# Performance work log

Measured on AMD Instinct MI355X. Metric: run time of the kernel, lower is better.

## Reference

```python
import jax, jax.numpy as jnp
import numpy as np

D_MODEL, D_K, D_V, D_H, SEQ = 1024, 64, 64, 16, 4096


def setup_inputs() -> dict:
    key = jax.random.key(0)
    ks = jax.random.split(key, 16)
    s = lambda fan_in: 1.0 / np.sqrt(fan_in)
    return {
        "X": jax.random.normal(ks[0], (SEQ, D_MODEL), jnp.float32),
        # shared Q/K/V projections (nn.Linear stores weight as [out, in])
        "Wq": jax.random.uniform(ks[1], (D_K, D_MODEL), jnp.float32, -s(D_MODEL), s(D_MODEL)),
        "bq": jax.random.uniform(ks[2], (D_K,), jnp.float32, -s(D_MODEL), s(D_MODEL)),
        "Wk": jax.random.uniform(ks[3], (D_K, D_MODEL), jnp.float32, -s(D_MODEL), s(D_MODEL)),
        "bk": jax.random.uniform(ks[4], (D_K,), jnp.float32, -s(D_MODEL), s(D_MODEL)),
        "Wv": jax.random.uniform(ks[5], (D_V, D_MODEL), jnp.float32, -s(D_MODEL), s(D_MODEL)),
        "bv": jax.random.uniform(ks[6], (D_V,), jnp.float32, -s(D_MODEL), s(D_MODEL)),
        # per-head linears stacked along head axis
        "Whq": jax.random.uniform(ks[7], (D_H, D_K, D_K), jnp.float32, -s(D_K), s(D_K)),
        "bhq": jax.random.uniform(ks[8], (D_H, D_K), jnp.float32, -s(D_K), s(D_K)),
        "Whk": jax.random.uniform(ks[9], (D_H, D_K, D_K), jnp.float32, -s(D_K), s(D_K)),
        "bhk": jax.random.uniform(ks[10], (D_H, D_K), jnp.float32, -s(D_K), s(D_K)),
        "Whv": jax.random.uniform(ks[11], (D_H, D_V, D_V), jnp.float32, -s(D_V), s(D_V)),
        "bhv": jax.random.uniform(ks[12], (D_H, D_V), jnp.float32, -s(D_V), s(D_V)),
        # final projection: d_h*d_v -> d_model
        "Wo": jax.random.uniform(ks[13], (D_MODEL, D_H * D_V), jnp.float32, -s(D_H * D_V), s(D_H * D_V)),
        "bo": jax.random.uniform(ks[14], (D_MODEL,), jnp.float32, -s(D_H * D_V), s(D_H * D_V)),
    }


def reference(X, Wq, bq, Wk, bk, Wv, bv, Whq, bhq, Whk, bhk, Whv, bhv, Wo, bo):
    # shared projections: [T, d_k] / [T, d_v]
    Q = X @ Wq.T + bq
    K = X @ Wk.T + bk
    V = X @ Wv.T + bv
    # per-head linears, all heads at once: [H, T, d_k]
    qh = jnp.einsum("tk,hjk->htj", Q, Whq) + bhq[:, None, :]
    kh = jnp.einsum("tk,hjk->htj", K, Whk) + bhk[:, None, :]
    vh = jnp.einsum("tv,hjv->htj", V, Whv) + bhv[:, None, :]
    # scaled dot-product attention per head: [H, T, T]
    scale = 1.0 / jnp.sqrt(jnp.asarray(Q.shape[-1], X.dtype))
    attn = jax.nn.softmax(jnp.einsum("htk,hsk->hts", qh, kh) * scale, axis=-1)
    rep = jnp.einsum("hts,hsv->htv", attn, vh)  # [H, T, d_v]
    # hstack heads -> [T, H*d_v], then final projection
    concat = rep.transpose(1, 0, 2).reshape(X.shape[0], -1)
    return concat @ Wo.T + bo
```

## Files before the change

kernel.cpp:

```cpp
#include <hip/hip_runtime.h>

#define T 4096
#define DM 1024
#define DK 64
#define H 16

typedef short s8 __attribute__((ext_vector_type(8)));
typedef float f4 __attribute__((ext_vector_type(4)));
typedef unsigned short us4 __attribute__((ext_vector_type(4)));
typedef unsigned u32x4 __attribute__((ext_vector_type(4)));
typedef __bf16 bf2 __attribute__((ext_vector_type(2)));

#define MFMA16(a,b,c) __builtin_amdgcn_mfma_f32_16x16x32_bf16((a),(b),(c),0,0,0)
#define SCALE_Q 0.18033688011112042f

__device__ __forceinline__ unsigned short f2bf(float x){
  __bf16 b = (__bf16)x;
  return __builtin_bit_cast(unsigned short, b);
}
__device__ __forceinline__ unsigned pk2(float a, float b){
  bf2 v; v[0] = (__bf16)a; v[1] = (__bf16)b;
  return __builtin_bit_cast(unsigned, v);
}

__device__ __forceinline__ void gload16(const void* g, void* lds){
  __builtin_amdgcn_global_load_lds((const __attribute__((address_space(1))) unsigned int*)g,
                                   (__attribute__((address_space(3))) unsigned int*)lds,
                                   16, 0, 0);
}

__device__ __forceinline__ void xch(unsigned X, unsigned Y, unsigned &E, unsigned &O){
#if __has_builtin(__builtin_amdgcn_permlane32_swap) && __has_builtin(__builtin_amdgcn_permlane16_swap)
  auto a = __builtin_amdgcn_permlane32_swap(X, Y, false, false);
  auto b = __builtin_amdgcn_permlane16_swap(a[0], a[1], false, false);
  E = b[0]; O = b[1];
#else
  int l = threadIdx.x & 63;
  int idxE = ((((l >> 4) & 1) * 32 + (l & 15))) << 2;
  unsigned eX = __builtin_amdgcn_ds_bpermute(idxE, X);
  unsigned eY = __builtin_amdgcn_ds_bpermute(idxE, Y);
  E = (l < 32) ? eX : eY;
  unsigned oX = __builtin_amdgcn_ds_bpermute(idxE + 64, X);
  unsigned oY = __builtin_amdgcn_ds_bpermute(idxE + 64, Y);
  O = (l < 32) ? oX : oY;
#endif
}

__global__ void cvt_bf16(const float* __restrict__ in, unsigned short* __restrict__ out, int n4){
  int i = blockIdx.x * blockDim.x + threadIdx.x;
  if (i >= n4) return;
  float4 v = reinterpret_cast<const float4*>(in)[i];
  us4 o;
  o[0] = f2bf(v.x); o[1] = f2bf(v.y); o[2] = f2bf(v.z); o[3] = f2bf(v.w);
  reinterpret_cast<us4*>(out)[i] = o;
}

#define N_WOB (DM * DM / 4)
#define N_W3  (64 * DM / 4)
#define N_WH  (16 * 64 * 64 / 4)
__global__ __launch_bounds__(256) void prep_all(
    const float* __restrict__ Wo,
    const float* __restrict__ Wq, const float* __restrict__ Wk, const float* __restrict__ Wv,
    const float* __restrict__ Whq, const float* __restrict__ Whk, const float* __restrict__ Whv,
    const float* __restrict__ bq, const float* __restrict__ bk, const float* __restrict__ bv,
    const float* __restrict__ bhq, const float* __restrict__ bhk, const float* __restrict__ bhv,
    unsigned short* __restrict__ Wob, unsigned short* __restrict__ W3b,
    unsigned short* __restrict__ Whb, float* __restrict__ beff){
  int idx = blockIdx.x * 256 + threadIdx.x;
  if (idx < N_WOB){
    float4 v = reinterpret_cast<const float4*>(Wo)[idx];
    us4 o; o[0]=f2bf(v.x); o[1]=f2bf(v.y); o[2]=f2bf(v.z); o[3]=f2bf(v.w);
    reinterpret_cast<us4*>(Wob)[idx] = o;
    return;
  }
  idx -= N_WOB;
  if (idx < 3 * N_W3){
    int seg = idx / N_W3, i = idx - seg * N_W3;
    const float* src = (seg == 0) ? Wq : ((seg == 1) ? Wk : Wv);
    float4 v = reinterpret_cast<const float4*>(src)[i];
    us4 o; o[0]=f2bf(v.x); o[1]=f2bf(v.y); o[2]=f2bf(v.z); o[3]=f2bf(v.w);
    reinterpret_cast<us4*>(W3b)[seg * N_W3 + i] = o;
    return;
  }
  idx -= 3 * N_W3;
  if (idx < 3 * N_WH){
    int seg = idx / N_WH, i = idx - seg * N_WH;
    const float* src = (seg == 0) ? Whq : ((seg == 1) ? Whk : Whv);
    float s = (seg == 0) ? SCALE_Q : 1.0f;
    float4 v = reinterpret_cast<const float4*>(src)[i];
    us4 o; o[0]=f2bf(v.x*s); o[1]=f2bf(v.y*s); o[2]=f2bf(v.z*s); o[3]=f2bf(v.w*s);
    reinterpret_cast<us4*>(Whb)[seg * N_WH + i] = o;
    return;
  }
  idx -= 3 * N_WH;
  if (idx < 3072){
    int seg = idx >> 10, j = idx & 1023;
    const float* Wh = (seg == 0) ? Whq : ((seg == 1) ? Whk : Whv);
    const float* b  = (seg == 0) ? bq  : ((seg == 1) ? bk  : bv);
    const float* bh = (seg == 0) ? bhq : ((seg == 1) ? bhk : bhv);
    float s = (seg == 0) ? SCALE_Q : 1.0f;
    const float* wr = Wh + j * 64;
    float acc = 0.f;
    #pragma unroll 8
    for (int k = 0; k < 64; ++k) acc += wr[k] * b[k];
    beff[idx] = (acc + bh[j]) * s;
  }
}

template<int MODE, int BM, int BN, int NT>
__global__ __launch_bounds__(256) void gemmX(const unsigned short* __restrict__ A,
                       const unsigned short* __restrict__ B,
                       const float* __restrict__ bias,
                       unsigned short* __restrict__ q_out,
                       unsigned short* __restrict__ k_out,
                       unsigned short* __restrict__ v_out,
                       float* __restrict__ f_out){
  __shared__ __align__(16) short la[2][BM * 64];
  __shared__ __align__(16) short lb[2][BN * 64];
  const int tid = threadIdx.x;
  const int wv = tid >> 6, l = tid & 63;
  const int lr = l & 15, lh = l >> 4;
  const int wr = wv >> 1, wc = wv & 1;
  const int tm = blockIdx.x / NT, tn = blockIdx.x % NT;
  const int t0 = tm * BM, o0 = tn * BN;
  constexpr int MF = BM / 32;
  constexpr int NF = BN / 32;
  constexpr int ACH = BM / 32;
  constexpr int BCH = BN / 32;
  constexpr int LAB = BM * 128;
  constexpr int LBB = BN * 128;

  f4 acc[MF][NF];
  #pragma unroll
  for (int i = 0; i < MF; ++i)
    #pragma unroll
    for (int j = 0; j < NF; ++j) acc[i][j] = (f4){0.f, 0.f, 0.f, 0.f};

  const int srow = tid >> 3;
  const int scs  = (tid & 7) ^ (srow & 7);
  const unsigned short* ap = A + (size_t)(t0 + srow) * DM + scs * 8;
  const unsigned short* bp = B + (size_t)(o0 + srow) * DM + scs * 8;
  char* ad = (char*)&la[0][0] + tid * 16;
  char* bd = (char*)&lb[0][0] + tid * 16;

  auto stage = [&](int BUF){
    #pragma unroll
    for (int i = 0; i < ACH; ++i)
      gload16(ap + (size_t)i * 32 * DM, ad + BUF * LAB + i * 4096);
    #pragma unroll
    for (int i = 0; i < BCH; ++i)
      gload16(bp + (size_t)i * 32 * DM, bd + BUF * LBB + i * 4096);
    ap += 64; bp += 64;
  };

  const int asw0 = (lh ^ (lr & 7)) * 16, asw1 = ((lh ^ 4) ^ (lr & 7)) * 16;
  const char* aB0 = (const char*)&la[0][0] + (wr * (BM / 2) + lr) * 128 + asw0;
  const char* aB1 = (const char*)&la[0][0] + (wr * (BM / 2) + lr) * 128 + asw1;
  const char* bB0 = (const char*)&lb[0][0] + (wc * (BN / 2) + lr) * 128 + asw0;
  const char* bB1 = (const char*)&lb[0][0] + (wc * (BN / 2) + lr) * 128 + asw1;

  auto step = [&](int BUF, bool dostage){
    if (dostage) stage(BUF ^ 1);
    s8 af[MF][2], bfr[NF][2];
    #pragma unroll
    for (int mf = 0; mf < MF; ++mf){
      af[mf][0] = *(const s8*)(aB0 + BUF * LAB + mf * 2048);
      af[mf][1] = *(const s8*)(aB1 + BUF * LAB + mf * 2048);
    }
    #pragma unroll
    for (int nf = 0; nf < NF; ++nf){
      bfr[nf][0] = *(const s8*)(bB0 + BUF * LBB + nf * 2048);
      bfr[nf][1] = *(const s8*)(bB1 + BUF * LBB + nf * 2048);
    }
    __builtin_amdgcn_s_setprio(1);
    #pragma unroll
    for (int mf = 0; mf < MF; ++mf)
      #pragma unroll
      for (int nf = 0; nf < NF; ++nf){
        acc[mf][nf] = MFMA16(af[mf][0], bfr[nf][0], acc[mf][nf]);
        acc[mf][nf] = MFMA16(af[mf][1], bfr[nf][1], acc[mf][nf]);
      }
    __builtin_amdgcn_s_setprio(0);
    __syncthreads();
  };

  stage(0);
  __syncthreads();
  #pragma unroll 1
  for (int t2 = 0; t2 < 8; ++t2){
    step(0, true);
    step(1, t2 < 7);
  }

  #pragma unroll
  for (int nf = 0; nf < NF; ++nf){
    int o = o0 + wc * (BN / 2) + nf * 16 + lr;
    float bs = (MODE == 4) ? 0.f : bias[o];
    int sel = o >> 6, oc = o & 63;
    unsigned short* yo = (sel == 0) ? q_out : ((sel == 1) ? k_out : v_out);
    #pragma unroll
    for (int mf = 0; mf < MF; ++mf)
      #pragma unroll
      for (int r = 0; r < 4; ++r){
        int t = t0 + wr * (BM / 2) + mf * 16 + lh * 4 + r;
        float v = acc[mf][nf][r] + bs;
        if (MODE == 2) f_out[(size_t)t * DM + o] = v;
        else           yo[(size_t)t * 64 + oc] = f2bf(v);
      }
  }
}

__global__ __launch_bounds__(256) void gemm_heads(const unsigned short* __restrict__ Yq,
                        const unsigned short* __restrict__ Yk,
                        const unsigned short* __restrict__ Yv,
                        const unsigned short* __restrict__ Whb,
                        const float* __restrict__ beff,
                        unsigned short* __restrict__ qhb,
                        unsigned short* __restrict__ khb,
                        unsigned short* __restrict__ vtb){
  const int tid = threadIdx.x;
  const int wv = tid >> 6, l = tid & 63;
  const int lr = l & 15, lh = l >> 4;
  const int rem = blockIdx.x % 48, tb = blockIdx.x / 48;
  const int kind = rem >> 4, h = rem & 15;
  const unsigned short* Y = (kind == 0) ? Yq : ((kind == 1) ? Yk : Yv);
  const unsigned short* B = Whb + (size_t)rem * 4096;
  const int t0 = tb * 256 + wv * 64;

  s8 wf[4][2], yf[4][2];
  #pragma unroll
  for (int nf = 0; nf < 4; ++nf)
    #pragma unroll
    for (int hf = 0; hf < 2; ++hf)
      wf[nf][hf] = *reinterpret_cast<const s8*>(B + (size_t)(nf * 16 + lr) * 64 + hf * 32 + lh * 8);
  #pragma unroll
  for (int mf = 0; mf < 4; ++mf)
    #pragma unroll
    for (int hf = 0; hf < 2; ++hf)
      yf[mf][hf] = *reinterpret_cast<const s8*>(Y + (size_t)(t0 + mf * 16 + lr) * 64 + hf * 32 + lh * 8);

  f4 acc[4][4];
  #pragma unroll
  for (int i = 0; i < 4; ++i)
    #pragma unroll
    for (int j = 0; j < 4; ++j) acc[i][j] = (f4){0.f, 0.f, 0.f, 0.f};

  if (kind < 2){
    #pragma unroll
    for (int mf = 0; mf < 4; ++mf)
      #pragma unroll
      for (int nf = 0; nf < 4; ++nf){
        acc[mf][nf] = MFMA16(yf[mf][0], wf[nf][0], acc[mf][nf]);
        acc[mf][nf] = MFMA16(yf[mf][1], wf[nf][1], acc[mf][nf]);
      }
    unsigned short* out = (kind == 0) ? qhb : khb;
    #pragma unroll
    for (int nf = 0; nf < 4; ++nf){
      int j = nf * 16 + lr;
      float bs = beff[rem * 64 + j];
      #pragma unroll
      for (int mf = 0; mf < 4; ++mf)
        #pragma unroll
        for (int r = 0; r < 4; ++r){
          int t = t0 + mf * 16 + lh * 4 + r;
          out[((size_t)h * T + t) * DK + j] = f2bf(acc[mf][nf][r] + bs);
        }
    }
  } else {
    #pragma unroll
    for (int nf = 0; nf < 4; ++nf)
      #pragma unroll
      for (int mf = 0; mf < 4; ++mf){
        acc[nf][mf] = MFMA16(wf[nf][0], yf[mf][0], acc[nf][mf]);
        acc[nf][mf] = MFMA16(wf[nf][1], yf[mf][1], acc[nf][mf]);
      }
    #pragma unroll
    for (int nf = 0; nf < 4; ++nf){
      float4 bsv = *reinterpret_cast<const float4*>(beff + rem * 64 + nf * 16 + lh * 4);
      #pragma unroll
      for (int r = 0; r < 4; ++r){
        int j = nf * 16 + lh * 4 + r;
        float bs = (r == 0) ? bsv.x : ((r == 1) ? bsv.y : ((r == 2) ? bsv.z : bsv.w));
        #pragma unroll
        for (int mf = 0; mf < 4; ++mf){
          int t = t0 + mf * 16 + lr;
          vtb[((size_t)h * DK + j) * T + t] = f2bf(acc[nf][mf][r] + bs);
        }
      }
    }
  }
}

__global__ __launch_bounds__(256) void attn_fwd(const unsigned short* __restrict__ qh,
                         const unsigned short* __restrict__ kh,
                         const unsigned short* __restrict__ vt,
                         float* __restrict__ Op, float* __restrict__ lv){
  __shared__ __align__(16) short lk[2][64 * 64];
  __shared__ __align__(16) short lv_[2][64 * 64];
  const int tid = threadIdx.x;
  const int wv = tid >> 6, l = tid & 63;
  const int lr = l & 15, lh = l >> 4;
  const int h = blockIdx.x >> 6;
  const int qblk = (blockIdx.x >> 1) & 31;
  const int half = blockIdx.x & 1;
  const int Q0 = qblk * 128 + wv * 32;
  const int S0 = half * (T / 2);

  s8 qf[2][2];
  #pragma unroll
  for (int qb = 0; qb < 2; ++qb)
    #pragma unroll
    for (int hf = 0; hf < 2; ++hf)
      qf[qb][hf] = *reinterpret_cast<const s8*>(
          qh + ((size_t)h * T + Q0 + qb * 16 + lr) * DK + hf * 32 + lh * 8);

  float ls[2] = {0.f, 0.f};
  f4 oa[2][4];
  #pragma unroll
  for (int qb = 0; qb < 2; ++qb)
    #pragma unroll
    for (int jb = 0; jb < 4; ++jb) oa[qb][jb] = (f4){0.f, 0.f, 0.f, 0.f};

  const int srow = tid >> 3;
  const int scs  = (tid & 7) ^ (srow & 7);
  const unsigned short* kp = kh + (size_t)h * T * DK + (size_t)S0 * DK + srow * DK + scs * 8;
  const unsigned short* vp = vt + (size_t)h * DK * T + S0 + srow * T + scs * 8;
  char* kd = (char*)&lk[0][0] + tid * 16;
  char* vd = (char*)&lv_[0][0] + tid * 16;

  auto stage = [&](int BUF){
    gload16(kp,           kd + BUF * 8192);
    gload16(kp + 32 * DK, kd + BUF * 8192 + 4096);
    gload16(vp,           vd + BUF * 8192);
    gload16(vp + 32 * T,  vd + BUF * 8192 + 4096);
    kp += 64 * DK; vp += 64;
  };

  const int sw0 = (lh ^ (lr & 7)) * 16, sw1 = ((lh ^ 4) ^ (lr & 7)) * 16;
  const char* kB0 = (const char*)&lk[0][0] + lr * 128 + sw0;
  const char* kB1 = (const char*)&lk[0][0] + lr * 128 + sw1;
  const char* vB0 = (const char*)&lv_[0][0] + lr * 128 + sw0;
  const char* vB1 = (const char*)&lv_[0][0] + lr * 128 + sw1;

  auto step = [&](int BUF, bool dostage){
    if (dostage) stage(BUF ^ 1);
    s8 kf[4][2], vf[4][2];
    #pragma unroll
    for (int mt = 0; mt < 4; ++mt){
      kf[mt][0] = *(const s8*)(kB0 + BUF * 8192 + mt * 2048);
      kf[mt][1] = *(const s8*)(kB1 + BUF * 8192 + mt * 2048);
      vf[mt][0] = *(const s8*)(vB0 + BUF * 8192 + mt * 2048);
      vf[mt][1] = *(const s8*)(vB1 + BUF * 8192 + mt * 2048);
    }
    #pragma unroll
    for (int qb = 0; qb < 2; ++qb){
      f4 sc[4];
      __builtin_amdgcn_s_setprio(1);
      #pragma unroll
      for (int mt = 0; mt < 4; ++mt){
        f4 z = (f4){0.f, 0.f, 0.f, 0.f};
        z = MFMA16(kf[mt][0], qf[qb][0], z);
        z = MFMA16(kf[mt][1], qf[qb][1], z);
        sc[mt] = z;
      }
      __builtin_amdgcn_s_setprio(0);
      float p[4][4];
      float rs0 = 0.f, rs1 = 0.f;
      #pragma unroll
      for (int mt = 0; mt < 4; ++mt){
        p[mt][0] = __builtin_amdgcn_exp2f(sc[mt][0]);
        p[mt][1] = __builtin_amdgcn_exp2f(sc[mt][1]);
        p[mt][2] = __builtin_amdgcn_exp2f(sc[mt][2]);
        p[mt][3] = __builtin_amdgcn_exp2f(sc[mt][3]);
        rs0 += p[mt][0] + p[mt][1];
        rs1 += p[mt][2] + p[mt][3];
      }
      ls[qb] += rs0 + rs1;
      unsigned w00 = pk2(p[0][0], p[0][1]), w01 = pk2(p[0][2], p[0][3]);
      unsigned w10 = pk2(p[1][0], p[1][1]), w11 = pk2(p[1][2], p[1][3]);
      unsigned w20 = pk2(p[2][0], p[2][1]), w21 = pk2(p[2][2], p[2][3]);
      unsigned w30 = pk2(p[3][0], p[3][1]), w31 = pk2(p[3][2], p[3][3]);
      unsigned e0, o0x, e1, o1x, e2, o2x, e3, o3x;
      xch(w00, w10, e0, o0x);
      xch(w01, w11, e1, o1x);
      xch(w20, w30, e2, o2x);
      xch(w21, w31, e3, o3x);
      u32x4 pa0u = {e0, e1, o0x, o1x};
      u32x4 pa1u = {e2, e3, o2x, o3x};
      s8 pa0 = __builtin_bit_cast(s8, pa0u);
      s8 pa1 = __builtin_bit_cast(s8, pa1u);
      __builtin_amdgcn_s_setprio(1);
      #pragma unroll
      for (int jb = 0; jb < 4; ++jb){
        oa[qb][jb] = MFMA16(pa0, vf[jb][0], oa[qb][jb]);
        oa[qb][jb] = MFMA16(pa1, vf[jb][1], oa[qb][jb]);
      }
      __builtin_amdgcn_s_setprio(0);
    }
    __syncthreads();
  };

  stage(0);
  __syncthreads();
  #pragma unroll 1
  for (int t2 = 0; t2 < 16; ++t2){
    step(0, true);
    step(1, t2 < 15);
  }

  const size_t base = (size_t)(half * H + h) * T;
  #pragma unroll
  for (int qb = 0; qb < 2; ++qb){
    float lq = ls[qb];
    lq += __shfl_xor(lq, 16);
    lq += __shfl_xor(lq, 32);
    if (lh == 0) lv[base + Q0 + qb * 16 + lr] = lq;
    #pragma unroll
    for (int r = 0; r < 4; ++r){
      size_t row = base + Q0 + qb * 16 + lh * 4 + r;
      #pragma unroll
      for (int jb = 0; jb < 4; ++jb)
        Op[(row << 6) + jb * 16 + lr] = oa[qb][jb][r];
    }
  }
}

__global__ __launch_bounds__(256) void attn_combine(const float* __restrict__ Op,
                              const float* __restrict__ lv,
                              unsigned short* __restrict__ cat){
  int idx = blockIdx.x * 256 + threadIdx.x;
  int c4 = idx & 15;
  int t = (idx >> 4) & (T - 1);
  int h = idx >> 16;
  size_t r0 = (size_t)h * T + t;
  size_t r1 = (size_t)(H + h) * T + t;
  float inv = 1.f / (lv[r0] + lv[r1]);
  float4 a = reinterpret_cast<const float4*>(Op)[(r0 << 4) + c4];
  float4 b = reinterpret_cast<const float4*>(Op)[(r1 << 4) + c4];
  us4 o;
  o[0] = f2bf((a.x + b.x) * inv);
  o[1] = f2bf((a.y + b.y) * inv);
  o[2] = f2bf((a.z + b.z) * inv);
  o[3] = f2bf((a.w + b.w) * inv);
  *reinterpret_cast<us4*>(&cat[(size_t)t * DM + h * DK + c4 * 4]) = o;
}

extern "C" void kernel_launch(void* const* d_in, const int* in_sizes, int n_in,
                              void* d_out, int out_size, void* d_ws, size_t ws_size,
                              hipStream_t stream){
  const float* X   = (const float*)d_in[0];
  const float* Wq  = (const float*)d_in[1];
  const float* bq  = (const float*)d_in[2];
  const float* Wk  = (const float*)d_in[3];
  const float* bk  = (const float*)d_in[4];
  const float* Wv  = (const float*)d_in[5];
  const float* bv  = (const float*)d_in[6];
  const float* Whq = (const float*)d_in[7];
  const float* bhq = (const float*)d_in[8];
  const float* Whk = (const float*)d_in[9];
  const float* bhk = (const float*)d_in[10];
  const float* Whv = (const float*)d_in[11];
  const float* bhv = (const float*)d_in[12];
  const float* Wo  = (const float*)d_in[13];
  const float* bo  = (const float*)d_in[14];

  char* w = (char*)d_ws;
  size_t off = 0;
  auto alloc = [&](size_t bytes) -> char* {
    char* p = w + off;
    off = (off + bytes + 255) & ~(size_t)255;
    return p;
  };
  unsigned short* Xbf = (unsigned short*)alloc((size_t)T * DM * 2);
  unsigned short* Wob = (unsigned short*)alloc((size_t)DM * DM * 2);
  unsigned short* W3b = (unsigned short*)alloc((size_t)192 * DM * 2);
  unsigned short* Whb = (unsigned short*)alloc((size_t)48 * 64 * 64 * 2);
  float* beff = (float*)alloc(48 * 64 * 4);
  unsigned short* Yq  = (unsigned short*)alloc((size_t)T * 64 * 2);
  unsigned short* Yk  = (unsigned short*)alloc((size_t)T * 64 * 2);
  unsigned short* Yv  = (unsigned short*)alloc((size_t)T * 64 * 2);
  unsigned short* qhb = (unsigned short*)alloc((size_t)H * T * DK * 2);
  unsigned short* khb = (unsigned short*)alloc((size_t)H * T * DK * 2);
  unsigned short* vtb = (unsigned short*)alloc((size_t)H * T * DK * 2);
  float* Oparts = (float*)alloc((size_t)2 * H * T * DK * 4);
  float* lvals  = (float*)alloc((size_t)2 * H * T * 4);
  unsigned short* cat = Xbf;

  cvt_bf16<<<(T * DM / 4) / 256, 256, 0, stream>>>(X, Xbf, T * DM / 4);
  {
    int total = N_WOB + 3 * N_W3 + 3 * N_WH + 3072;
    prep_all<<<(total + 255) / 256, 256, 0, stream>>>(
        Wo, Wq, Wk, Wv, Whq, Whk, Whv, bq, bk, bv, bhq, bhk, bhv,
        Wob, W3b, Whb, beff);
  }

  gemmX<4, 64, 64, 3><<<(T / 64) * 3, 256, 0, stream>>>(Xbf, W3b, nullptr, Yq, Yk, Yv, nullptr);

  gemm_heads<<<(T / 256) * 48, 256, 0, stream>>>(Yq, Yk, Yv, Whb, beff, qhb, khb, vtb);

  attn_fwd<<<(T / 128) * H * 2, 256, 0, stream>>>(qhb, khb, vtb, Oparts, lvals);
  attn_combine<<<(H * T * 16) / 256, 256, 0, stream>>>(Oparts, lvals, cat);

  gemmX<2, 128, 64, 16><<<(T / 128) * 16, 256, 0, stream>>>(cat, Wob, bo, nullptr, nullptr, nullptr, (float*)d_out);
}
```

Before: 151.6 us.

## Switch attention to 32x32 MFMA tiles and drop split-KV combine kernel

Rewrites the attention kernel to use 32x32x16 bf16 MFMA instead of 16x16x32, so each wave handles 32 query rows with fewer, larger matrix ops and a single permlane32 swap instead of a two-stage lane exchange. The key dimension is no longer split across two blocks; each block walks all 4096 keys and normalizes and writes bf16 output directly, which removes the fp32 partial buffers and the separate combine kernel. The cost is half as many blocks (512 instead of 1024), which lowers parallelism and gives each block a longer serial loop.

```diff
diff --git a/kernel.cpp b/kernel.cpp
--- a/kernel.cpp
+++ b/kernel.cpp
@@ -7,11 +7,14 @@
 
 typedef short s8 __attribute__((ext_vector_type(8)));
 typedef float f4 __attribute__((ext_vector_type(4)));
+typedef float f16v __attribute__((ext_vector_type(16)));
 typedef unsigned short us4 __attribute__((ext_vector_type(4)));
+typedef unsigned u32x2 __attribute__((ext_vector_type(2)));
 typedef unsigned u32x4 __attribute__((ext_vector_type(4)));
 typedef __bf16 bf2 __attribute__((ext_vector_type(2)));
 
 #define MFMA16(a,b,c) __builtin_amdgcn_mfma_f32_16x16x32_bf16((a),(b),(c),0,0,0)
+#define MFMA32(a,b,c) __builtin_amdgcn_mfma_f32_32x32x16_bf16((a),(b),(c),0,0,0)
 #define SCALE_Q 0.18033688011112042f
 
 __device__ __forceinline__ unsigned short f2bf(float x){
@@ -29,20 +32,18 @@
                                    16, 0, 0);
 }
 
-__device__ __forceinline__ void xch(unsigned X, unsigned Y, unsigned &E, unsigned &O){
-#if __has_builtin(__builtin_amdgcn_permlane32_swap) && __has_builtin(__builtin_amdgcn_permlane16_swap)
+__device__ __forceinline__ void swp(unsigned X, unsigned Y, unsigned &E, unsigned &O){
+#if __has_builtin(__builtin_amdgcn_permlane32_swap)
   auto a = __builtin_amdgcn_permlane32_swap(X, Y, false, false);
-  auto b = __builtin_amdgcn_permlane16_swap(a[0], a[1], false, false);
-  E = b[0]; O = b[1];
+  E = a[0]; O = a[1];
 #else
   int l = threadIdx.x & 63;
-  int idxE = ((((l >> 4) & 1) * 32 + (l & 15))) << 2;
-  unsigned eX = __builtin_amdgcn_ds_bpermute(idxE, X);
-  unsigned eY = __builtin_amdgcn_ds_bpermute(idxE, Y);
-  E = (l < 32) ? eX : eY;
-  unsigned oX = __builtin_amdgcn_ds_bpermute(idxE + 64, X);
-  unsigned oY = __builtin_amdgcn_ds_bpermute(idxE + 64, Y);
-  O = (l < 32) ? oX : oY;
+  unsigned sx = __builtin_amdgcn_ds_bpermute(((l & 31) << 2), X);
+  unsigned sy = __builtin_amdgcn_ds_bpermute(((l & 31) << 2), Y);
+  unsigned hx = __builtin_amdgcn_ds_bpermute((((l & 31) + 32) << 2), X);
+  unsigned hy = __builtin_amdgcn_ds_bpermute((((l & 31) + 32) << 2), Y);
+  E = (l < 32) ? sx : sy;
+  O = (l < 32) ? hx : hy;
 #endif
 }
 
@@ -294,155 +295,140 @@
 __global__ __launch_bounds__(256) void attn_fwd(const unsigned short* __restrict__ qh,
                          const unsigned short* __restrict__ kh,
                          const unsigned short* __restrict__ vt,
-                         float* __restrict__ Op, float* __restrict__ lv){
-  __shared__ __align__(16) short lk[2][64 * 64];
-  __shared__ __align__(16) short lv_[2][64 * 64];
+                         unsigned short* __restrict__ cat){
+  __shared__ __align__(16) char ldsb[2][16384];
   const int tid = threadIdx.x;
   const int wv = tid >> 6, l = tid & 63;
-  const int lr = l & 15, lh = l >> 4;
-  const int h = blockIdx.x >> 6;
-  const int qblk = (blockIdx.x >> 1) & 31;
-  const int half = blockIdx.x & 1;
-  const int Q0 = qblk * 128 + wv * 32;
-  const int S0 = half * (T / 2);
-
-  s8 qf[2][2];
-  #pragma unroll
-  for (int qb = 0; qb < 2; ++qb)
-    #pragma unroll
-    for (int hf = 0; hf < 2; ++hf)
-      qf[qb][hf] = *reinterpret_cast<const s8*>(
-          qh + ((size_t)h * T + Q0 + qb * 16 + lr) * DK + hf * 32 + lh * 8);
-
-  float ls[2] = {0.f, 0.f};
-  f4 oa[2][4];
-  #pragma unroll
-  for (int qb = 0; qb < 2; ++qb)
-    #pragma unroll
-    for (int jb = 0; jb < 4; ++jb) oa[qb][jb] = (f4){0.f, 0.f, 0.f, 0.f};
+  const int l31 = l & 31, h5 = l >> 5, l7 = l & 7;
+  const int h = blockIdx.x >> 5, qblk = blockIdx.x & 31;
+  const int Q0w = qblk * 128 + wv * 32;
+
+  s8 qf[4];
+  #pragma unroll
+  for (int kk = 0; kk < 4; ++kk)
+    qf[kk] = *reinterpret_cast<const s8*>(
+        qh + ((size_t)h * T + Q0w + l31) * DK + kk * 16 + h5 * 8);
+
+  float ls = 0.f;
+  f16v oa0, oa1;
+  #pragma unroll
+  for (int i = 0; i < 16; ++i){ oa0[i] = 0.f; oa1[i] = 0.f; }
 
   const int srow = tid >> 3;
   const int scs  = (tid & 7) ^ (srow & 7);
-  const unsigned short* kp = kh + (size_t)h * T * DK + (size_t)S0 * DK + srow * DK + scs * 8;
-  const unsigned short* vp = vt + (size_t)h * DK * T + S0 + srow * T + scs * 8;
-  char* kd = (char*)&lk[0][0] + tid * 16;
-  char* vd = (char*)&lv_[0][0] + tid * 16;
+  const unsigned short* kp = kh + (size_t)h * T * DK + srow * DK + scs * 8;
+  const unsigned short* vp = vt + (size_t)h * DK * T + srow * T + scs * 8;
+  char* sd = &ldsb[0][0] + tid * 16;
 
   auto stage = [&](int BUF){
-    gload16(kp,           kd + BUF * 8192);
-    gload16(kp + 32 * DK, kd + BUF * 8192 + 4096);
-    gload16(vp,           vd + BUF * 8192);
-    gload16(vp + 32 * T,  vd + BUF * 8192 + 4096);
+    gload16(kp,           sd + BUF * 16384);
+    gload16(kp + 32 * DK, sd + BUF * 16384 + 4096);
+    gload16(vp,           sd + BUF * 16384 + 8192);
+    gload16(vp + 32 * T,  sd + BUF * 16384 + 12288);
     kp += 64 * DK; vp += 64;
   };
 
-  const int sw0 = (lh ^ (lr & 7)) * 16, sw1 = ((lh ^ 4) ^ (lr & 7)) * 16;
-  const char* kB0 = (const char*)&lk[0][0] + lr * 128 + sw0;
-  const char* kB1 = (const char*)&lk[0][0] + lr * 128 + sw1;
-  const char* vB0 = (const char*)&lv_[0][0] + lr * 128 + sw0;
-  const char* vB1 = (const char*)&lv_[0][0] + lr * 128 + sw1;
+  const char* ba[2][4];
+  #pragma unroll
+  for (int t2 = 0; t2 < 2; ++t2)
+    #pragma unroll
+    for (int kk = 0; kk < 4; ++kk)
+      ba[t2][kk] = &ldsb[0][0] + (t2 * 32 + l31) * 128 + ((((kk << 1) | h5) ^ l7) << 4);
 
   auto step = [&](int BUF, bool dostage){
     if (dostage) stage(BUF ^ 1);
-    s8 kf[4][2], vf[4][2];
-    #pragma unroll
-    for (int mt = 0; mt < 4; ++mt){
-      kf[mt][0] = *(const s8*)(kB0 + BUF * 8192 + mt * 2048);
-      kf[mt][1] = *(const s8*)(kB1 + BUF * 8192 + mt * 2048);
-      vf[mt][0] = *(const s8*)(vB0 + BUF * 8192 + mt * 2048);
-      vf[mt][1] = *(const s8*)(vB1 + BUF * 8192 + mt * 2048);
-    }
-    #pragma unroll
-    for (int qb = 0; qb < 2; ++qb){
-      f4 sc[4];
-      __builtin_amdgcn_s_setprio(1);
-      #pragma unroll
-      for (int mt = 0; mt < 4; ++mt){
-        f4 z = (f4){0.f, 0.f, 0.f, 0.f};
-        z = MFMA16(kf[mt][0], qf[qb][0], z);
-        z = MFMA16(kf[mt][1], qf[qb][1], z);
-        sc[mt] = z;
-      }
-      __builtin_amdgcn_s_setprio(0);
-      float p[4][4];
-      float rs0 = 0.f, rs1 = 0.f;
-      #pragma unroll
-      for (int mt = 0; mt < 4; ++mt){
-        p[mt][0] = __builtin_amdgcn_exp2f(sc[mt][0]);
-        p[mt][1] = __builtin_amdgcn_exp2f(sc[mt][1]);
-        p[mt][2] = __builtin_amdgcn_exp2f(sc[mt][2]);
-        p[mt][3] = __builtin_amdgcn_exp2f(sc[mt][3]);
-        rs0 += p[mt][0] + p[mt][1];
-        rs1 += p[mt][2] + p[mt][3];
-      }
-      ls[qb] += rs0 + rs1;
-      unsigned w00 = pk2(p[0][0], p[0][1]), w01 = pk2(p[0][2], p[0][3]);
-      unsigned w10 = pk2(p[1][0], p[1][1]), w11 = pk2(p[1][2], p[1][3]);
-      unsigned w20 = pk2(p[2][0], p[2][1]), w21 = pk2(p[2][2], p[2][3]);
-      unsigned w30 = pk2(p[3][0], p[3][1]), w31 = pk2(p[3][2], p[3][3]);
-      unsigned e0, o0x, e1, o1x, e2, o2x, e3, o3x;
-      xch(w00, w10, e0, o0x);
-      xch(w01, w11, e1, o1x);
-      xch(w20, w30, e2, o2x);
-      xch(w21, w31, e3, o3x);
-      u32x4 pa0u = {e0, e1, o0x, o1x};
-      u32x4 pa1u = {e2, e3, o2x, o3x};
-      s8 pa0 = __builtin_bit_cast(s8, pa0u);
-      s8 pa1 = __builtin_bit_cast(s8, pa1u);
-      __builtin_amdgcn_s_setprio(1);
-      #pragma unroll
-      for (int jb = 0; jb < 4; ++jb){
-        oa[qb][jb] = MFMA16(pa0, vf[jb][0], oa[qb][jb]);
-        oa[qb][jb] = MFMA16(pa1, vf[jb][1], oa[qb][jb]);
-      }
-      __builtin_amdgcn_s_setprio(0);
-    }
+    s8 kf0[4], kf1[4];
+    #pragma unroll
+    for (int kk = 0; kk < 4; ++kk){
+      kf0[kk] = *(const s8*)(ba[0][kk] + BUF * 16384);
+      kf1[kk] = *(const s8*)(ba[1][kk] + BUF * 16384);
+    }
+    f16v sc0, sc1;
+    #pragma unroll
+    for (int i = 0; i < 16; ++i){ sc0[i] = 0.f; sc1[i] = 0.f; }
+    __builtin_amdgcn_s_setprio(1);
+    #pragma unroll
+    for (int kk = 0; kk < 4; ++kk) sc0 = MFMA32(kf0[kk], qf[kk], sc0);
+    #pragma unroll
+    for (int kk = 0; kk < 4; ++kk) sc1 = MFMA32(kf1[kk], qf[kk], sc1);
+    __builtin_amdgcn_s_setprio(0);
+    s8 vf0[4], vf1[4];
+    #pragma unroll
+    for (int p = 0; p < 4; ++p){
+      vf0[p] = *(const s8*)(ba[0][p] + BUF * 16384 + 8192);
+      vf1[p] = *(const s8*)(ba[1][p] + BUF * 16384 + 8192);
+    }
+    float p0[16], p1[16];
+    #pragma unroll
+    for (int i = 0; i < 16; ++i){
+      p0[i] = __builtin_amdgcn_exp2f(sc0[i]);
+      p1[i] = __builtin_amdgcn_exp2f(sc1[i]);
+    }
+    float r0 = (p0[0]+p0[1]) + (p0[2]+p0[3]);
+    float r1 = (p0[4]+p0[5]) + (p0[6]+p0[7]);
+    float r2 = (p0[8]+p0[9]) + (p0[10]+p0[11]);
+    float r3 = (p0[12]+p0[13]) + (p0[14]+p0[15]);
+    float r4 = (p1[0]+p1[1]) + (p1[2]+p1[3]);
+    float r5 = (p1[4]+p1[5]) + (p1[6]+p1[7]);
+    float r6 = (p1[8]+p1[9]) + (p1[10]+p1[11]);
+    float r7 = (p1[12]+p1[13]) + (p1[14]+p1[15]);
+    ls += ((r0+r1)+(r2+r3)) + ((r4+r5)+(r6+r7));
+    unsigned a0 = pk2(p0[0],p0[1]),  a1 = pk2(p0[2],p0[3]);
+    unsigned a2 = pk2(p0[4],p0[5]),  a3 = pk2(p0[6],p0[7]);
+    unsigned a4 = pk2(p0[8],p0[9]),  a5 = pk2(p0[10],p0[11]);
+    unsigned a6 = pk2(p0[12],p0[13]), a7 = pk2(p0[14],p0[15]);
+    unsigned b0 = pk2(p1[0],p1[1]),  b1 = pk2(p1[2],p1[3]);
+    unsigned b2 = pk2(p1[4],p1[5]),  b3 = pk2(p1[6],p1[7]);
+    unsigned b4 = pk2(p1[8],p1[9]),  b5 = pk2(p1[10],p1[11]);
+    unsigned b6 = pk2(p1[12],p1[13]), b7 = pk2(p1[14],p1[15]);
+    unsigned e0,o0, e1,o1, e2,o2, e3,o3, e4,o4, e5,o5, e6,o6, e7,o7;
+    swp(a0, a2, e0, o0);  swp(a1, a3, e1, o1);
+    swp(a4, a6, e2, o2);  swp(a5, a7, e3, o3);
+    swp(b0, b2, e4, o4);  swp(b1, b3, e5, o5);
+    swp(b4, b6, e6, o6);  swp(b5, b7, e7, o7);
+    u32x4 pu0 = {e0, e1, o0, o1};
+    u32x4 pu1 = {e2, e3, o2, o3};
+    u32x4 pu2 = {e4, e5, o4, o5};
+    u32x4 pu3 = {e6, e7, o6, o7};
+    s8 pa0 = __builtin_bit_cast(s8, pu0);
+    s8 pa1 = __builtin_bit_cast(s8, pu1);
+    s8 pa2 = __builtin_bit_cast(s8, pu2);
+    s8 pa3 = __builtin_bit_cast(s8, pu3);
+    __builtin_amdgcn_s_setprio(1);
+    oa0 = MFMA32(vf0[0], pa0, oa0);
+    oa0 = MFMA32(vf0[1], pa1, oa0);
+    oa0 = MFMA32(vf0[2], pa2, oa0);
+    oa0 = MFMA32(vf0[3], pa3, oa0);
+    oa1 = MFMA32(vf1[0], pa0, oa1);
+    oa1 = MFMA32(vf1[1], pa1, oa1);
+    oa1 = MFMA32(vf1[2], pa2, oa1);
+    oa1 = MFMA32(vf1[3], pa3, oa1);
+    __builtin_amdgcn_s_setprio(0);
     __syncthreads();
   };
 
   stage(0);
   __syncthreads();
   #pragma unroll 1
-  for (int t2 = 0; t2 < 16; ++t2){
+  for (int it = 0; it < 32; ++it){
     step(0, true);
-    step(1, t2 < 15);
-  }
-
-  const size_t base = (size_t)(half * H + h) * T;
-  #pragma unroll
-  for (int qb = 0; qb < 2; ++qb){
-    float lq = ls[qb];
-    lq += __shfl_xor(lq, 16);
-    lq += __shfl_xor(lq, 32);
-    if (lh == 0) lv[base + Q0 + qb * 16 + lr] = lq;
-    #pragma unroll
-    for (int r = 0; r < 4; ++r){
-      size_t row = base + Q0 + qb * 16 + lh * 4 + r;
-      #pragma unroll
-      for (int jb = 0; jb < 4; ++jb)
-        Op[(row << 6) + jb * 16 + lr] = oa[qb][jb][r];
-    }
-  }
-}
-
-__global__ __launch_bounds__(256) void attn_combine(const float* __restrict__ Op,
-                              const float* __restrict__ lv,
-                              unsigned short* __restrict__ cat){
-  int idx = blockIdx.x * 256 + threadIdx.x;
-  int c4 = idx & 15;
-  int t = (idx >> 4) & (T - 1);
-  int h = idx >> 16;
-  size_t r0 = (size_t)h * T + t;
-  size_t r1 = (size_t)(H + h) * T + t;
-  float inv = 1.f / (lv[r0] + lv[r1]);
-  float4 a = reinterpret_cast<const float4*>(Op)[(r0 << 4) + c4];
-  float4 b = reinterpret_cast<const float4*>(Op)[(r1 << 4) + c4];
-  us4 o;
-  o[0] = f2bf((a.x + b.x) * inv);
-  o[1] = f2bf((a.y + b.y) * inv);
-  o[2] = f2bf((a.z + b.z) * inv);
-  o[3] = f2bf((a.w + b.w) * inv);
-  *reinterpret_cast<us4*>(&cat[(size_t)t * DM + h * DK + c4 * 4]) = o;
+    step(1, it < 31);
+  }
+
+  float lq = ls + __shfl_xor(ls, 32);
+  float inv = 1.f / lq;
+  const int t = Q0w + l31;
+  unsigned short* crow = cat + (size_t)t * DM + h * DK;
+  #pragma unroll
+  for (int g = 0; g < 4; ++g){
+    u32x2 w0, w1;
+    w0[0] = pk2(oa0[g*4+0] * inv, oa0[g*4+1] * inv);
+    w0[1] = pk2(oa0[g*4+2] * inv, oa0[g*4+3] * inv);
+    w1[0] = pk2(oa1[g*4+0] * inv, oa1[g*4+1] * inv);
+    w1[1] = pk2(oa1[g*4+2] * inv, oa1[g*4+3] * inv);
+    *reinterpret_cast<u32x2*>(crow + g * 8 + h5 * 4)      = w0;
+    *reinterpret_cast<u32x2*>(crow + 32 + g * 8 + h5 * 4) = w1;
+  }
 }
 
 extern "C" void kernel_launch(void* const* d_in, const int* in_sizes, int n_in,
@@ -482,8 +468,6 @@
   unsigned short* qhb = (unsigned short*)alloc((size_t)H * T * DK * 2);
   unsigned short* khb = (unsigned short*)alloc((size_t)H * T * DK * 2);
   unsigned short* vtb = (unsigned short*)alloc((size_t)H * T * DK * 2);
-  float* Oparts = (float*)alloc((size_t)2 * H * T * DK * 4);
-  float* lvals  = (float*)alloc((size_t)2 * H * T * 4);
   unsigned short* cat = Xbf;
 
   cvt_bf16<<<(T * DM / 4) / 256, 256, 0, stream>>>(X, Xbf, T * DM / 4);
@@ -498,8 +482,7 @@
 
   gemm_heads<<<(T / 256) * 48, 256, 0, stream>>>(Yq, Yk, Yv, Whb, beff, qhb, khb, vtb);
 
-  attn_fwd<<<(T / 128) * H * 2, 256, 0, stream>>>(qhb, khb, vtb, Oparts, lvals);
-  attn_combine<<<(H * T * 16) / 256, 256, 0, stream>>>(Oparts, lvals, cat);
+  attn_fwd<<<(T / 128) * H, 256, 0, stream>>>(qhb, khb, vtb, cat);
 
   gemmX<2, 128, 64, 16><<<(T / 128) * 16, 256, 0, stream>>>(cat, Wob, bo, nullptr, nullptr, nullptr, (float*)d_out);
 }
```

Result: faster. 143.4 us (-5.4%).
